# Optimization experiments

Measured on AMD Instinct MI355X. Metric: run time of the kernel, lower is better.

Reference implementation:

```python
import jax, jax.numpy as jnp
import numpy as np

NG, ND, NS, E, DIM, H = 20000, 8000, 8000, 300000, 256, 8
HD = DIM // H
SCALE = 1.0 / float(np.sqrt(HD))
EPS = 1e-5


def _ln(x, g, b):
    mu = x.mean(-1, keepdims=True)
    var = ((x - mu) ** 2).mean(-1, keepdims=True)
    return (x - mu) / jnp.sqrt(var + EPS) * g + b


def _attn(h_src, h_dst, Wq, bq, Wk, bk, Wv, bv, src, dst, n_dst):
    # multi-head edge dot-product attention with edge_softmax over incoming edges
    Q = (h_dst @ Wq.T + bq).reshape(-1, H, HD)
    K = (h_src @ Wk.T + bk).reshape(-1, H, HD)
    V = (h_src @ Wv.T + bv).reshape(-1, H, HD)
    score = jnp.einsum('ehd,ehd->eh', K[src], Q[dst]) * SCALE  # [E, H]
    m = jax.ops.segment_max(score, dst, num_segments=n_dst)
    m = jnp.where(jnp.isfinite(m), m, 0.0)  # nodes with no in-edges
    a = jnp.exp(score - m[dst])
    denom = jax.ops.segment_sum(a, dst, num_segments=n_dst)
    a = a / denom[dst]
    h = jax.ops.segment_sum(V[src] * a[:, :, None], dst, num_segments=n_dst)
    return h.reshape(n_dst, DIM)


def _bahdanau(m1, m2, W1, b1, W2, b2, v, bv):
    e1 = (jnp.tanh(m1 @ W1.T + b1) @ v.T + bv)[:, 0]
    e2 = (jnp.tanh(m2 @ W2.T + b2) @ v.T + bv)[:, 0]
    w = jax.nn.softmax(jnp.stack([e1, e2], axis=1), axis=1)
    return w[:, 0:1] * m1 + w[:, 1:2] * m2


def _forward(gene_feat, drug_feat, disease_feat,
             dg_Wq, dg_bq, dg_Wk, dg_bk, dg_Wv, dg_bv,
             disg_Wq, disg_bq, disg_Wk, disg_bk, disg_Wv, disg_bv,
             gd_Wq, gd_bq, gd_Wk, gd_bk, gd_Wv, gd_bv,
             gdis_Wq, gdis_bq, gdis_Wk, gdis_bk, gdis_Wv, gdis_bv,
             f_W1, f_b1, f_W2, f_b2, f_v, f_bv,
             ln1_g, ln1_b, ln2_g, ln2_b,
             dg_src, dg_dst, disg_src, disg_dst, gd_src, gd_dst, gdis_src, gdis_dst):
    gm_drug = _attn(drug_feat, gene_feat, dg_Wq, dg_bq, dg_Wk, dg_bk, dg_Wv, dg_bv, dg_src, dg_dst, NG)
    gm_dis = _attn(disease_feat, gene_feat, disg_Wq, disg_bq, disg_Wk, disg_bk, disg_Wv, disg_bv, disg_src, disg_dst, NG)
    has_d = jnp.zeros((NG,), bool).at[dg_dst].set(True)
    has_s = jnp.zeros((NG,), bool).at[disg_dst].set(True)
    fused = _bahdanau(gm_drug, gm_dis, f_W1, f_b1, f_W2, f_b2, f_v, f_bv)
    gene_msg = jnp.where((has_d & has_s)[:, None], fused,
                         jnp.where(has_d[:, None], gm_drug,
                                   jnp.where(has_s[:, None], gm_dis, 0.0)))
    gene_out = _ln(gene_feat + jax.nn.gelu(gene_msg, approximate=False), ln1_g, ln1_b)
    drug_msg = _attn(gene_out, drug_feat, gd_Wq, gd_bq, gd_Wk, gd_bk, gd_Wv, gd_bv, gd_src, gd_dst, ND)
    dis_msg = _attn(gene_out, disease_feat, gdis_Wq, gdis_bq, gdis_Wk, gdis_bk, gdis_Wv, gdis_bv, gdis_src, gdis_dst, NS)
    drug_out = _ln(drug_feat + jax.nn.gelu(drug_msg, approximate=False), ln2_g, ln2_b)
    disease_out = _ln(disease_feat + jax.nn.gelu(dis_msg, approximate=False), ln2_g, ln2_b)
    return (drug_out, disease_out, gene_out)


def setup_inputs() -> dict:
    ks = jax.random.split(jax.random.key(0), 40)
    it = iter(range(40))

    def nrm(shape):
        return jax.random.normal(ks[next(it)], shape, dtype=jnp.float32)

    def xav(din, dout):
        lim = float(np.sqrt(6.0 / (din + dout)))
        return jax.random.uniform(ks[next(it)], (dout, din), minval=-lim, maxval=lim, dtype=jnp.float32)

    def ridx(n, hi):
        return jax.random.randint(ks[next(it)], (n,), 0, hi, dtype=jnp.int32)

    inp = {}
    inp['gene_feat'] = nrm((NG, DIM))
    inp['drug_feat'] = nrm((ND, DIM))
    inp['disease_feat'] = nrm((NS, DIM))
    for p in ['dg', 'disg', 'gd', 'gdis']:
        inp[p + '_Wq'] = xav(DIM, DIM)
        inp[p + '_bq'] = jnp.zeros((DIM,), jnp.float32)
        inp[p + '_Wk'] = xav(DIM, DIM)
        inp[p + '_bk'] = jnp.zeros((DIM,), jnp.float32)
        inp[p + '_Wv'] = xav(DIM, DIM)
        inp[p + '_bv'] = jnp.zeros((DIM,), jnp.float32)
    inp['f_W1'] = xav(DIM, DIM); inp['f_b1'] = jnp.zeros((DIM,), jnp.float32)
    inp['f_W2'] = xav(DIM, DIM); inp['f_b2'] = jnp.zeros((DIM,), jnp.float32)
    inp['f_v'] = xav(DIM, 1); inp['f_bv'] = jnp.zeros((1,), jnp.float32)
    inp['ln1_g'] = jnp.ones((DIM,), jnp.float32); inp['ln1_b'] = jnp.zeros((DIM,), jnp.float32)
    inp['ln2_g'] = jnp.ones((DIM,), jnp.float32); inp['ln2_b'] = jnp.zeros((DIM,), jnp.float32)
    inp['dg_src'] = ridx(E, ND); inp['dg_dst'] = ridx(E, NG)
    inp['disg_src'] = ridx(E, NS); inp['disg_dst'] = ridx(E, NG)
    inp['gd_src'] = ridx(E, NG); inp['gd_dst'] = ridx(E, ND)
    inp['gdis_src'] = ridx(E, NG); inp['gdis_dst'] = ridx(E, NS)
    return inp


def reference(gene_feat, drug_feat, disease_feat,
              dg_Wq, dg_bq, dg_Wk, dg_bk, dg_Wv, dg_bv,
              disg_Wq, disg_bq, disg_Wk, disg_bk, disg_Wv, disg_bv,
              gd_Wq, gd_bq, gd_Wk, gd_bk, gd_Wv, gd_bv,
              gdis_Wq, gdis_bq, gdis_Wk, gdis_bk, gdis_Wv, gdis_bv,
              f_W1, f_b1, f_W2, f_b2, f_v, f_bv,
              ln1_g, ln1_b, ln2_g, ln2_b,
              dg_src, dg_dst, disg_src, disg_dst, gd_src, gd_dst, gdis_src, gdis_dst):
    return _forward(gene_feat, drug_feat, disease_feat,
                    dg_Wq, dg_bq, dg_Wk, dg_bk, dg_Wv, dg_bv,
                    disg_Wq, disg_bq, disg_Wk, disg_bk, disg_Wv, disg_bv,
                    gd_Wq, gd_bq, gd_Wk, gd_bk, gd_Wv, gd_bv,
                    gdis_Wq, gdis_bq, gdis_Wk, gdis_bk, gdis_Wv, gdis_bv,
                    f_W1, f_b1, f_W2, f_b2, f_v, f_bv,
                    ln1_g, ln1_b, ln2_g, ln2_b,
                    dg_src, dg_dst, disg_src, disg_dst, gd_src, gd_dst, gdis_src, gdis_dst)
```

## Files before the change

### kernel.cpp

```cpp
#include <hip/hip_runtime.h>

#define NG 20000
#define ND 8000
#define NS 8000
#define EE 300000
#define DIM 256
#define SCALE_QK 0.17677669529663687f
#define LNEPS 1e-5f

#define MAXB 40
#define L1CH 2048
#define NCH1 ((EE + L1CH - 1) / L1CH)
#define CB_G 8704
#define CB_S 10496
#define RB_G (40 * CB_G)
#define RB_S (32 * CB_S)

typedef __attribute__((ext_vector_type(4))) float floatx4;
typedef __attribute__((ext_vector_type(8))) short shortx8;
typedef __attribute__((ext_vector_type(8))) unsigned short ushortx8;
typedef unsigned int u32;

__device__ __forceinline__ float bf2f(unsigned short u) {
    union { unsigned u; float f; } c; c.u = ((unsigned)u) << 16; return c.f;
}
__device__ __forceinline__ unsigned short f2bf(float f) {
    union { float f; unsigned u; } c; c.f = f;
    return (unsigned short)((c.u + 0x7fffu + ((c.u >> 16) & 1u)) >> 16);
}
__device__ __forceinline__ float gelu_exact(float v) {
    return 0.5f * v * (1.0f + erff(v * 0.70710678118654752f));
}

__device__ __forceinline__ void async_load16(const unsigned short* g,
                                             unsigned short* lds) {
    __builtin_amdgcn_global_load_lds(
        (const __attribute__((address_space(1))) u32*)(const void*)g,
        (__attribute__((address_space(3))) u32*)(void*)lds, 16, 0, 0);
}

__device__ __forceinline__ int swzoff(int row, int q) {
    int p = (row >> 1) & 7, b = row & 1;
    return ((row >> 4) * 64 + p * 8 + (((b << 2) + q) ^ p)) * 8;
}

struct GemmDesc {
    const unsigned short* A; const unsigned short* W;
    const float* b1; const float* b2; const float* b3; const float* b4;
    unsigned short* C; int ldc;
    const float* vvec; float* evec;
    int M; int gx; int ncol; int mode; int kvi;
};
struct GemmBatch { GemmDesc d[4]; };

__global__ __launch_bounds__(256, 4) void gemm_batch_kernel(GemmBatch gb)
{
    __shared__ unsigned short As[2][128 * 32];
    __shared__ unsigned short Bs[2][64 * 32];
    const GemmDesc d = gb.d[blockIdx.z];
    if ((int)blockIdx.x >= d.gx) return;
    const int n0 = blockIdx.y * 64;
    if (n0 >= d.ncol) return;

    const int tid = threadIdx.x;
    const int lane = tid & 63, wv = tid >> 6;
    const int quad = lane >> 4, l16 = lane & 15;
    const int m0 = blockIdx.x * 128;

    const int sp = lane >> 3, ss = lane & 7;
    const int srow = 2 * sp + ((ss ^ sp) >> 2);
    const int sq = (ss ^ sp) & 3;
    const unsigned short* gA0 = d.A + (size_t)(m0 + wv * 16 + srow) * 256 + sq * 8;
    const unsigned short* gA1 = d.A + (size_t)(m0 + 64 + wv * 16 + srow) * 256 + sq * 8;
    const unsigned short* gB  = d.W + (size_t)(n0 + wv * 16 + srow) * 256 + sq * 8;

    floatx4 acc[2][4];
#pragma unroll
    for (int i = 0; i < 2; ++i)
#pragma unroll
        for (int j = 0; j < 4; ++j) acc[i][j] = (floatx4){0.f, 0.f, 0.f, 0.f};

    async_load16(gA0, &As[0][(wv * 16) * 32]);
    async_load16(gA1, &As[0][(64 + wv * 16) * 32]);
    async_load16(gB,  &Bs[0][(wv * 16) * 32]);
    __syncthreads();

    for (int k0 = 0; k0 < 256; k0 += 32) {
        const int buf = (k0 >> 5) & 1;
        if (k0 < 224) {
            const int nb = buf ^ 1;
            async_load16(gA0 + k0 + 32, &As[nb][(wv * 16) * 32]);
            async_load16(gA1 + k0 + 32, &As[nb][(64 + wv * 16) * 32]);
            async_load16(gB + k0 + 32,  &Bs[nb][(wv * 16) * 32]);
        }
        shortx8 af[2], bfr[4];
#pragma unroll
        for (int mf = 0; mf < 2; ++mf)
            af[mf] = *(const shortx8*)(&As[buf][swzoff(wv * 32 + mf * 16 + l16, quad)]);
#pragma unroll
        for (int nf = 0; nf < 4; ++nf)
            bfr[nf] = *(const shortx8*)(&Bs[buf][swzoff(nf * 16 + l16, quad)]);
#pragma unroll
        for (int mf = 0; mf < 2; ++mf)
#pragma unroll
            for (int nf = 0; nf < 4; ++nf)
                acc[mf][nf] = __builtin_amdgcn_mfma_f32_16x16x32_bf16(
                    af[mf], bfr[nf], acc[mf][nf], 0, 0, 0);
        __syncthreads();
    }

    if (d.mode == 0) {
#pragma unroll
        for (int mf = 0; mf < 2; ++mf)
#pragma unroll
            for (int r = 0; r < 4; ++r) {
                int m = m0 + wv * 32 + mf * 16 + quad * 4 + r;
                if (m < d.M) {
#pragma unroll
                    for (int nf = 0; nf < 4; ++nf) {
                        int n = n0 + nf * 16 + l16;
                        int h = n >> 8;
                        const float* bp = (h == 0) ? d.b1 : (h == 1) ? d.b2
                                        : (h == 2) ? d.b3 : d.b4;
                        float bn = bp[n & 255];
                        int pos;
                        if (d.kvi) {
                            int nn = n & 511;
                            pos = (n & ~511) + ((nn & 255) >> 2) * 8 + (nn & 3) +
                                  ((nn >> 8) << 2);
                        } else {
                            pos = n;
                        }
                        d.C[(size_t)m * d.ldc + pos] = f2bf(acc[mf][nf][r] + bn);
                    }
                }
            }
    } else {
        float p[2][4] = {};
#pragma unroll
        for (int mf = 0; mf < 2; ++mf)
#pragma unroll
            for (int nf = 0; nf < 4; ++nf) {
                int n = n0 + nf * 16 + l16;
                float vn = d.vvec[n];
                float bn = d.b1[n];
#pragma unroll
                for (int r = 0; r < 4; ++r)
                    p[mf][r] += vn * tanhf(acc[mf][nf][r] + bn);
            }
#pragma unroll
        for (int mf = 0; mf < 2; ++mf)
#pragma unroll
            for (int r = 0; r < 4; ++r) {
                float s = p[mf][r];
                s += __shfl_xor(s, 1); s += __shfl_xor(s, 2);
                s += __shfl_xor(s, 4); s += __shfl_xor(s, 8);
                if (l16 == 0) {
                    int m = m0 + wv * 32 + mf * 16 + quad * 4 + r;
                    if (m < d.M) atomicAdd(&d.evec[m], s);
                }
            }
    }
}

struct PrepP {
    int* zb; int zn; int nzb;
    const float* wsrc[14];
    unsigned short* wout;
    const float* gf; const float* df; const float* sf;
    unsigned short* go; unsigned short* dfo; unsigned short* so;
};
__global__ void prep_kernel(PrepP p) {
    int bid = blockIdx.x, tid = threadIdx.x;
    if (bid < p.nzb) {
        int i = bid * 256 + tid;
        if (i < p.zn) p.zb[i] = 0;
        return;
    }
    bid -= p.nzb;
    if (bid < 896) {
        int idx = bid * 256 + tid;
        int mat = idx >> 14;
        int e = (idx & 16383) << 2;
        float4 f = *(const float4*)(p.wsrc[mat] + e);
        ushort4 t;
        t.x = f2bf(f.x); t.y = f2bf(f.y); t.z = f2bf(f.z); t.w = f2bf(f.w);
        *(ushort4*)(p.wout + ((size_t)mat << 16) + e) = t;
        return;
    }
    bid -= 896;
    const int NG4 = NG * 64, ND4 = ND * 64, NS4 = NS * 64;
    int i = bid * 256 + tid;
    const float* in; unsigned short* out; int j;
    if (i < NG4) { in = p.gf; out = p.go; j = i; }
    else if (i < NG4 + ND4) { in = p.df; out = p.dfo; j = i - NG4; }
    else if (i < NG4 + ND4 + NS4) { in = p.sf; out = p.so; j = i - NG4 - ND4; }
    else return;
    float4 f = *(const float4*)(in + (size_t)j * 4);
    ushort4 t;
    t.x = f2bf(f.x); t.y = f2bf(f.y); t.z = f2bf(f.z); t.w = f2bf(f.w);
    *(ushort4*)(out + (size_t)j * 4) = t;
}

__global__ void fillf_kernel(float* __restrict__ p, int n, float v) {
    int i = blockIdx.x * blockDim.x + threadIdx.x;
    if (i < n) p[i] = v;
}

struct L1P {
    const int* src[4];
    const int* dst[4];
    int* brec[4];
    int* bcur;
};
__global__ __launch_bounds__(256) void l1_bucket_kernel(L1P a) {
    __shared__ int hist[MAXB];
    int g = blockIdx.x / NCH1, c = blockIdx.x - g * NCH1;
    int base = c * L1CH;
    int tid = threadIdx.x;
    const int shift = (g < 2) ? 9 : 8;
    const int CB = (g < 2) ? CB_G : CB_S;
    const int NB = (g < 2) ? 40 : 32;
    if (tid < NB) hist[tid] = 0;
    __syncthreads();
    const int* __restrict__ dstp = a.dst[g];
    const int* __restrict__ srcp = a.src[g];
    int bk[8], rec[8], lr[8];
#pragma unroll
    for (int j = 0; j < 8; ++j) {
        int e = base + j * 256 + tid;
        bool ok = e < EE;
        int dd = ok ? dstp[e] : 0;
        int ss = ok ? srcp[e] : 0;
        bk[j] = dd >> shift;
        rec[j] = ((dd & ((1 << shift) - 1)) << 15) | ss;
        lr[j] = ok ? atomicAdd(&hist[bk[j]], 1) : -1;
    }
    __syncthreads();
    if (tid < NB) {
        int h = hist[tid];
        if (h > 0) hist[tid] = atomicAdd(&a.bcur[g * MAXB + tid], h);
    }
    __syncthreads();
    int* __restrict__ recp = a.brec[g];
#pragma unroll
    for (int j = 0; j < 8; ++j) {
        if (lr[j] >= 0) {
            int pos = hist[bk[j]] + lr[j];
            if (pos < CB) recp[bk[j] * CB + pos] = rec[j];
        }
    }
}

struct L2P {
    const int* brec[4];
    const int* bcur;
    int* cnt[4];
    int* offs[4];
    int* srcs[4];
};
__global__ __launch_bounds__(256) void l2_csr_kernel(L2P a) {
    __shared__ int hist[512];
    __shared__ int loffs[512];
    __shared__ int cur[512];
    __shared__ int ws2[4];
    __shared__ int bb;
    int bid = blockIdx.x, tid = threadIdx.x;
    int g, b;
    if (bid < 40) { g = 0; b = bid; }
    else if (bid < 80) { g = 1; b = bid - 40; }
    else if (bid < 112) { g = 2; b = bid - 80; }
    else { g = 3; b = bid - 112; }
    const int shift = (g < 2) ? 9 : 8;
    const int BSZ = 1 << shift;
    const int CB = (g < 2) ? CB_G : CB_S;
    const int N = (g < 2) ? NG : ((g == 2) ? ND : NS);
    hist[tid] = 0; hist[256 + tid] = 0;
    if (tid == 0) {
        int s = 0;
        const int* bc = a.bcur + g * MAXB;
        for (int i = 0; i < b; ++i) s += bc[i];
        bb = s;
    }
    __syncthreads();
    int total = a.bcur[g * MAXB + b];
    if (total > CB) total = CB;
    const int* __restrict__ recp = a.brec[g] + b * CB;
    for (int i = tid; i < total; i += 256)
        atomicAdd(&hist[recp[i] >> 15], 1);
    __syncthreads();
    int v0 = hist[2 * tid], v1 = hist[2 * tid + 1];
    int s = v0 + v1, x = s;
    int lane = tid & 63, wv = tid >> 6;
#pragma unroll
    for (int o = 1; o < 64; o <<= 1) {
        int u = __shfl_up(x, o);
        if (lane >= o) x += u;
    }
    if (lane == 63) ws2[wv] = x;
    __syncthreads();
    int woff = 0;
    for (int w = 0; w < wv; ++w) woff += ws2[w];
    int excl = woff + x - s;
    loffs[2 * tid] = excl; loffs[2 * tid + 1] = excl + v0;
    cur[2 * tid] = excl;  cur[2 * tid + 1] = excl + v0;
    int base = bb;
    int lo = b << shift;
    for (int i = tid; i < BSZ; i += 256) {
        int dd = lo + i;
        if (dd < N) {
            a.cnt[g][dd] = hist[i];
            a.offs[g][dd] = base + loffs[i];
        }
    }
    __syncthreads();
    int* __restrict__ sp = a.srcs[g];
    for (int i = tid; i < total; i += 256) {
        int rec = recp[i];
        int pos = atomicAdd(&cur[rec >> 15], 1);
        sp[base + pos] = rec & 0x7fff;
    }
}

__device__ __forceinline__ void wave_attn_node(
    const unsigned short* __restrict__ Q, int qs,
    const unsigned short* __restrict__ KV,
    const int* __restrict__ offs, const int* __restrict__ cnt,
    const int* __restrict__ srcs, int du, int lane,
    float& g0, float& g1, float& g2, float& g3)
{
    const int lo = lane * 4;
    const int lofs = lane * 8;
    ushort4 qv = *(const ushort4*)(Q + (size_t)du * qs + lo);
    const float q0 = bf2f(qv.x), q1 = bf2f(qv.y), q2 = bf2f(qv.z), q3 = bf2f(qv.w);
    const int beg = offs[du], num = cnt[du];

    float m[8], l[8], a[8][4];
#pragma unroll
    for (int c = 0; c < 8; ++c) {
        m[c] = -INFINITY; l[c] = 0.f;
        a[c][0] = a[c][1] = a[c][2] = a[c][3] = 0.f;
    }

    int sb[8];
    if (num > 0) {
#pragma unroll
        for (int c = 0; c < 8; ++c)
            sb[c] = srcs[beg + ((c < num) ? c : (num - 1))];
    }

    for (int i = 0; i < num; i += 8) {
        int sn[8];
        const bool more = (i + 8) < num;
        if (more) {
#pragma unroll
            for (int c = 0; c < 8; ++c) {
                int idx = i + 8 + c;
                sn[c] = srcs[beg + ((idx < num) ? idx : (num - 1))];
            }
        }
        ushortx8 kv[8];
#pragma unroll
        for (int c = 0; c < 8; ++c)
            kv[c] = *(const ushortx8*)(KV + (size_t)sb[c] * 512 + lofs);
        float p[8];
#pragma unroll
        for (int c = 0; c < 8; ++c)
            p[c] = q0 * bf2f(kv[c][0]) + q1 * bf2f(kv[c][1]) +
                   q2 * bf2f(kv[c][2]) + q3 * bf2f(kv[c][3]);
#pragma unroll
        for (int c = 0; c < 8; ++c) p[c] += __shfl_xor(p[c], 1);
#pragma unroll
        for (int c = 0; c < 8; ++c) p[c] += __shfl_xor(p[c], 2);
#pragma unroll
        for (int c = 0; c < 8; ++c) p[c] += __shfl_xor(p[c], 4);
#pragma unroll
        for (int c = 0; c < 8; ++c) {
            if (i + c < num) {
                float sc = p[c] * SCALE_QK;
                float mn = fmaxf(m[c], sc);
                float eo = __expf(m[c] - mn);
                float en = __expf(sc - mn);
                a[c][0] = a[c][0] * eo + en * bf2f(kv[c][4]);
                a[c][1] = a[c][1] * eo + en * bf2f(kv[c][5]);
                a[c][2] = a[c][2] * eo + en * bf2f(kv[c][6]);
                a[c][3] = a[c][3] * eo + en * bf2f(kv[c][7]);
                l[c] = l[c] * eo + en;
                m[c] = mn;
            }
        }
        if (more) {
#pragma unroll
            for (int c = 0; c < 8; ++c) sb[c] = sn[c];
        }
    }

    float ms = fmaxf(fmaxf(fmaxf(m[0], m[1]), fmaxf(m[2], m[3])),
                     fmaxf(fmaxf(m[4], m[5]), fmaxf(m[6], m[7])));
    float A0 = 0.f, A1 = 0.f, A2 = 0.f, A3 = 0.f, L = 0.f;
    if (ms > -INFINITY) {
#pragma unroll
        for (int c = 0; c < 8; ++c) {
            float w = __expf(m[c] - ms);
            A0 += a[c][0] * w; A1 += a[c][1] * w;
            A2 += a[c][2] * w; A3 += a[c][3] * w;
            L += l[c] * w;
        }
    }
    float inv = (L > 0.f) ? 1.f / L : 0.f;
    g0 = A0 * inv; g1 = A1 * inv; g2 = A2 * inv; g3 = A3 * inv;
}

__device__ __forceinline__ void wave_ln_store(
    float x0, float x1, float x2, float x3,
    const float* __restrict__ g, const float* __restrict__ b,
    float* __restrict__ out, unsigned short* __restrict__ out_bf,
    int du, int lo)
{
    float s1 = x0 + x1 + x2 + x3;
    float s2 = x0 * x0 + x1 * x1 + x2 * x2 + x3 * x3;
#pragma unroll
    for (int o = 1; o < 64; o <<= 1) {
        s1 += __shfl_xor(s1, o);
        s2 += __shfl_xor(s2, o);
    }
    float mu = s1 * (1.f / 256.f);
    float var = fmaxf(s2 * (1.f / 256.f) - mu * mu, 0.f);
    float rs = rsqrtf(var + LNEPS);
    float4 gv = *(const float4*)(g + lo);
    float4 bv = *(const float4*)(b + lo);
    float y0 = (x0 - mu) * rs * gv.x + bv.x;
    float y1 = (x1 - mu) * rs * gv.y + bv.y;
    float y2 = (x2 - mu) * rs * gv.z + bv.z;
    float y3 = (x3 - mu) * rs * gv.w + bv.w;
    *(float4*)(out + (size_t)du * 256 + lo) = make_float4(y0, y1, y2, y3);
    if (out_bf) {
        ushort4 t; t.x = f2bf(y0); t.y = f2bf(y1); t.z = f2bf(y2); t.w = f2bf(y3);
        *(ushort4*)(out_bf + (size_t)du * 256 + lo) = t;
    }
}

struct AggDesc {
    const unsigned short* Q; int qs;
    const unsigned short* KV;
    const int* offs; const int* cnt; const int* srcs;
    unsigned short* gm;
    const float* feat; const float* g; const float* b; float* out;
    int N;
};
template <int LN>
__global__ __launch_bounds__(256) void agg2_kernel(AggDesc a0, AggDesc a1, int nb0)
{
    const bool first = (int)blockIdx.x < nb0;
    const AggDesc d = first ? a0 : a1;
    const int bx = first ? blockIdx.x : (blockIdx.x - nb0);
    int lane = threadIdx.x & 63, wv = threadIdx.x >> 6;
    int nd = bx * 4 + wv;
    if (nd >= d.N) return;
    int du = __builtin_amdgcn_readfirstlane(nd);
    int lo = lane * 4;
    float g0, g1, g2, g3;
    wave_attn_node(d.Q, d.qs, d.KV, d.offs, d.cnt, d.srcs, du, lane, g0, g1, g2, g3);
    if (LN == 0) {
        ushort4 t; t.x = f2bf(g0); t.y = f2bf(g1); t.z = f2bf(g2); t.w = f2bf(g3);
        *(ushort4*)(d.gm + (size_t)du * 256 + lo) = t;
    } else {
        float4 fv = *(const float4*)(d.feat + (size_t)du * 256 + lo);
        float x0 = fv.x + gelu_exact(g0);
        float x1 = fv.y + gelu_exact(g1);
        float x2 = fv.z + gelu_exact(g2);
        float x3 = fv.w + gelu_exact(g3);
        wave_ln_store(x0, x1, x2, x3, d.g, d.b, d.out, nullptr, du, lo);
    }
}

__global__ __launch_bounds__(256) void gene_fusion_kernel(
    const float* __restrict__ gene_feat, const unsigned short* __restrict__ gm_d,
    const unsigned short* __restrict__ gm_s, const float* __restrict__ e1,
    const float* __restrict__ e2, const int* __restrict__ cnt_d,
    const int* __restrict__ cnt_s, const float* __restrict__ g,
    const float* __restrict__ b, float* __restrict__ out,
    unsigned short* __restrict__ out_bf)
{
    int lane = threadIdx.x & 63, wv = threadIdx.x >> 6;
    int d = blockIdx.x * 4 + wv;
    if (d >= NG) return;
    int du = __builtin_amdgcn_readfirstlane(d);
    int lo = lane * 4;
    ushort4 v1 = *(const ushort4*)(gm_d + (size_t)du * 256 + lo);
    ushort4 v2 = *(const ushort4*)(gm_s + (size_t)du * 256 + lo);
    bool hd = cnt_d[du] > 0, hs = cnt_s[du] > 0;
    float wa, wb;
    if (hd && hs) {
        float aa = e1[du], bb = e2[du];
        float mm = fmaxf(aa, bb);
        float ea = __expf(aa - mm), eb = __expf(bb - mm);
        float inv = 1.f / (ea + eb);
        wa = ea * inv; wb = eb * inv;
    } else if (hd) { wa = 1.f; wb = 0.f; }
    else if (hs) { wa = 0.f; wb = 1.f; }
    else { wa = 0.f; wb = 0.f; }
    float m0 = wa * bf2f(v1.x) + wb * bf2f(v2.x);
    float m1 = wa * bf2f(v1.y) + wb * bf2f(v2.y);
    float m2 = wa * bf2f(v1.z) + wb * bf2f(v2.z);
    float m3 = wa * bf2f(v1.w) + wb * bf2f(v2.w);
    float4 fv = *(const float4*)(gene_feat + (size_t)du * 256 + lo);
    float x0 = fv.x + gelu_exact(m0);
    float x1 = fv.y + gelu_exact(m1);
    float x2 = fv.z + gelu_exact(m2);
    float x3 = fv.w + gelu_exact(m3);
    wave_ln_store(x0, x1, x2, x3, g, b, out, out_bf, du, lo);
}

extern "C" void kernel_launch(void* const* d_in, const int* in_sizes, int n_in,
                              void* d_out, int out_size, void* d_ws, size_t ws_size,
                              hipStream_t stream)
{
    float* out_f32 = (float*)d_out;

    const float* gene_feat    = (const float*)d_in[0];
    const float* drug_feat    = (const float*)d_in[1];
    const float* disease_feat = (const float*)d_in[2];
    const float* dg_Wq = (const float*)d_in[3];
    const float* dg_bq = (const float*)d_in[4];
    const float* dg_Wk = (const float*)d_in[5];
    const float* dg_bk = (const float*)d_in[6];
    const float* dg_Wv = (const float*)d_in[7];
    const float* dg_bv = (const float*)d_in[8];
    const float* disg_Wq = (const float*)d_in[9];
    const float* disg_bq = (const float*)d_in[10];
    const float* disg_Wk = (const float*)d_in[11];
    const float* disg_bk = (const float*)d_in[12];
    const float* disg_Wv = (const float*)d_in[13];
    const float* disg_bv = (const float*)d_in[14];
    const float* gd_Wq = (const float*)d_in[15];
    const float* gd_bq = (const float*)d_in[16];
    const float* gd_Wk = (const float*)d_in[17];
    const float* gd_bk = (const float*)d_in[18];
    const float* gd_Wv = (const float*)d_in[19];
    const float* gd_bv = (const float*)d_in[20];
    const float* gdis_Wq = (const float*)d_in[21];
    const float* gdis_bq = (const float*)d_in[22];
    const float* gdis_Wk = (const float*)d_in[23];
    const float* gdis_bk = (const float*)d_in[24];
    const float* gdis_Wv = (const float*)d_in[25];
    const float* gdis_bv = (const float*)d_in[26];
    const float* f_W1 = (const float*)d_in[27];
    const float* f_b1 = (const float*)d_in[28];
    const float* f_W2 = (const float*)d_in[29];
    const float* f_b2 = (const float*)d_in[30];
    const float* f_v  = (const float*)d_in[31];
    const float* ln1_g = (const float*)d_in[33];
    const float* ln1_b = (const float*)d_in[34];
    const float* ln2_g = (const float*)d_in[35];
    const float* ln2_b = (const float*)d_in[36];
    const int* dg_src   = (const int*)d_in[37];
    const int* dg_dst   = (const int*)d_in[38];
    const int* disg_src = (const int*)d_in[39];
    const int* disg_dst = (const int*)d_in[40];
    const int* gd_src   = (const int*)d_in[41];
    const int* gd_dst   = (const int*)d_in[42];
    const int* gdis_src = (const int*)d_in[43];
    const int* gdis_dst = (const int*)d_in[44];

    char* ws = (char*)d_ws;
    size_t off = 0;
    auto alloc = [&](size_t bytes) -> char* {
        char* p = ws + off;
        off += (bytes + 511) & ~(size_t)511;
        return p;
    };
    int* bcur = (int*)alloc(4 * MAXB * 4);
    float* e1 = (float*)alloc(NG * 4);
    float* e2 = (float*)alloc(NG * 4);
    size_t zero_len = off;
    int* offs_dg   = (int*)alloc(NG * 4);
    int* offs_disg = (int*)alloc(NG * 4);
    int* offs_gd   = (int*)alloc(ND * 4);
    int* offs_gdis = (int*)alloc(NS * 4);
    int* cnt_dg    = (int*)alloc(NG * 4);
    int* cnt_disg  = (int*)alloc(NG * 4);
    int* cnt_gd    = (int*)alloc(ND * 4);
    int* cnt_gdis  = (int*)alloc(NS * 4);
    int* srcs_dg   = (int*)alloc((size_t)EE * 4);
    int* srcs_disg = (int*)alloc((size_t)EE * 4);
    int* srcs_gd   = (int*)alloc((size_t)EE * 4);
    int* srcs_gdis = (int*)alloc((size_t)EE * 4);
    unsigned short* Q12  = (unsigned short*)alloc((size_t)NG * 512 * 2);
    unsigned short* KVb  = (unsigned short*)alloc((size_t)NG * 512 * 2);
    unsigned short* gm_d = (unsigned short*)alloc((size_t)NG * 256 * 2);
    unsigned short* gm_s = (unsigned short*)alloc((size_t)NG * 256 * 2);
    unsigned short* gene_bf = (unsigned short*)alloc((size_t)NG * 256 * 2);
    unsigned short* drug_bf = (unsigned short*)alloc((size_t)ND * 256 * 2);
    unsigned short* dis_bf  = (unsigned short*)alloc((size_t)NS * 256 * 2);
    unsigned short* Wbf     = (unsigned short*)alloc((size_t)14 * 65536 * 2);
    char* guard = alloc(64 * 1024);
    (void)guard;
    size_t need = off;

    int* brec0 = (int*)Q12;
    int* brec1 = brec0 + RB_G;
    int* brec2 = brec1 + RB_G;
    int* brec3 = brec2 + RB_S;

    unsigned short* KVb2 = gm_s;
    unsigned short* KVs1b = KVb + (size_t)ND * 512;
    unsigned short* Qd = Q12;
    unsigned short* Qs = Q12 + (size_t)ND * 256;
    unsigned short* gene_out_bf = gm_d;

    float* out_drug = out_f32;
    float* out_dis  = out_drug + (size_t)ND * 256;
    float* out_gene = out_dis + (size_t)NS * 256;

    if (ws_size < need) {
        fillf_kernel<<<(out_size + 255) / 256, 256, 0, stream>>>(out_f32, out_size, 1000.0f);
        return;
    }

    {
        PrepP p;
        p.zb = (int*)d_ws;
        p.zn = (int)(zero_len / 4);
        p.nzb = (p.zn + 255) / 256;
        const float* wl[14] = {dg_Wq, disg_Wq, dg_Wk, dg_Wv, disg_Wk, disg_Wv,
                               gd_Wk, gd_Wv, gdis_Wk, gdis_Wv, gd_Wq, gdis_Wq,
                               f_W1, f_W2};
        for (int i = 0; i < 14; ++i) p.wsrc[i] = wl[i];
        p.wout = Wbf;
        p.gf = gene_feat; p.df = drug_feat; p.sf = disease_feat;
        p.go = gene_bf; p.dfo = drug_bf; p.so = dis_bf;
        int nfeat = ((NG + ND + NS) * 64 + 255) / 256;
        prep_kernel<<<p.nzb + 896 + nfeat, 256, 0, stream>>>(p);
    }

    {
        L1P p;
        p.src[0] = dg_src; p.src[1] = disg_src; p.src[2] = gd_src; p.src[3] = gdis_src;
        p.dst[0] = dg_dst; p.dst[1] = disg_dst; p.dst[2] = gd_dst; p.dst[3] = gdis_dst;
        p.brec[0] = brec0; p.brec[1] = brec1; p.brec[2] = brec2; p.brec[3] = brec3;
        p.bcur = bcur;
        l1_bucket_kernel<<<4 * NCH1, 256, 0, stream>>>(p);
    }
    {
        L2P p;
        p.brec[0] = brec0; p.brec[1] = brec1; p.brec[2] = brec2; p.brec[3] = brec3;
        p.bcur = bcur;
        p.cnt[0] = cnt_dg; p.cnt[1] = cnt_disg; p.cnt[2] = cnt_gd; p.cnt[3] = cnt_gdis;
        p.offs[0] = offs_dg; p.offs[1] = offs_disg; p.offs[2] = offs_gd; p.offs[3] = offs_gdis;
        p.srcs[0] = srcs_dg; p.srcs[1] = srcs_disg; p.srcs[2] = srcs_gd; p.srcs[3] = srcs_gdis;
        l2_csr_kernel<<<144, 256, 0, stream>>>(p);
    }

    const int GXG = (NG + 127) / 128;
    const int GXS = (ND + 127) / 128;

    auto mkd = [](const unsigned short* A, const unsigned short* W,
                  const float* b1, const float* b2, const float* b3, const float* b4,
                  unsigned short* C, int ldc, const float* vv, float* ev,
                  int M, int gx, int ncol, int mode, int kvi) {
        GemmDesc d;
        d.A = A; d.W = W; d.b1 = b1; d.b2 = b2; d.b3 = b3; d.b4 = b4;
        d.C = C; d.ldc = ldc; d.vvec = vv; d.evec = ev;
        d.M = M; d.gx = gx; d.ncol = ncol; d.mode = mode; d.kvi = kvi;
        return d;
    };
    auto mka = [](const unsigned short* Q, int qs, const unsigned short* KV,
                  const int* offs, const int* cnt, const int* srcs,
                  unsigned short* gm, const float* feat, const float* g,
                  const float* b, float* out, int N) {
        AggDesc d;
        d.Q = Q; d.qs = qs; d.KV = KV; d.offs = offs; d.cnt = cnt; d.srcs = srcs;
        d.gm = gm; d.feat = feat; d.g = g; d.b = b; d.out = out; d.N = N;
        return d;
    };

    {
        GemmBatch gb;
        gb.d[0] = mkd(gene_bf, Wbf, dg_bq, disg_bq, dg_bq, dg_bq,
                      Q12, 512, nullptr, nullptr, NG, GXG, 512, 0, 0);
        gb.d[1] = mkd(drug_bf, Wbf + (size_t)2 * 65536, dg_bk, dg_bv, dg_bk, dg_bk,
                      KVb, 512, nullptr, nullptr, ND, GXS, 512, 0, 1);
        gb.d[2] = mkd(dis_bf, Wbf + (size_t)4 * 65536, disg_bk, disg_bv, disg_bk, disg_bk,
                      KVs1b, 512, nullptr, nullptr, NS, GXS, 512, 0, 1);
        gb.d[3] = gb.d[2]; gb.d[3].gx = 0;
        gemm_batch_kernel<<<dim3(GXG, 8, 3), 256, 0, stream>>>(gb);
    }

    {
        AggDesc a0 = mka(Q12, 512, KVb, offs_dg, cnt_dg, srcs_dg,
                         gm_d, nullptr, nullptr, nullptr, nullptr, NG);
        AggDesc a1 = mka(Q12 + 256, 512, KVs1b, offs_disg, cnt_disg, srcs_disg,
                         gm_s, nullptr, nullptr, nullptr, nullptr, NG);
        int nb = (NG + 3) / 4;
        agg2_kernel<0><<<2 * nb, 256, 0, stream>>>(a0, a1, nb);
    }

    {
        GemmBatch gb;
        gb.d[0] = mkd(gm_d, Wbf + (size_t)12 * 65536, f_b1, f_b1, f_b1, f_b1,
                      nullptr, 256, f_v, e1, NG, GXG, 256, 1, 0);
        gb.d[1] = mkd(gm_s, Wbf + (size_t)13 * 65536, f_b2, f_b2, f_b2, f_b2,
                      nullptr, 256, f_v, e2, NG, GXG, 256, 1, 0);
        gb.d[2] = mkd(drug_bf, Wbf + (size_t)10 * 65536, gd_bq, gd_bq, gd_bq, gd_bq,
                      Qd, 256, nullptr, nullptr, ND, GXS, 256, 0, 0);
        gb.d[3] = mkd(dis_bf, Wbf + (size_t)11 * 65536, gdis_bq, gdis_bq, gdis_bq, gdis_bq,
                      Qs, 256, nullptr, nullptr, NS, GXS, 256, 0, 0);
        gemm_batch_kernel<<<dim3(GXG, 4, 4), 256, 0, stream>>>(gb);
    }

    gene_fusion_kernel<<<(NG + 3) / 4, 256, 0, stream>>>(
        gene_feat, gm_d, gm_s, e1, e2, cnt_dg, cnt_disg, ln1_g, ln1_b,
        out_gene, gene_out_bf);

    {
        GemmBatch gb;
        gb.d[0] = mkd(gene_out_bf, Wbf + (size_t)6 * 65536, gd_bk, gd_bv, gd_bk, gd_bk,
                      KVb, 512, nullptr, nullptr, NG, GXG, 512, 0, 1);
        gb.d[1] = mkd(gene_out_bf, Wbf + (size_t)8 * 65536, gdis_bk, gdis_bv, gdis_bk, gdis_bk,
                      KVb2, 512, nullptr, nullptr, NG, GXG, 512, 0, 1);
        gb.d[2] = gb.d[1]; gb.d[2].gx = 0;
        gb.d[3] = gb.d[1]; gb.d[3].gx = 0;
        gemm_batch_kernel<<<dim3(GXG, 8, 2), 256, 0, stream>>>(gb);
    }

    {
        AggDesc a0 = mka(Qd, 256, KVb, offs_gd, cnt_gd, srcs_gd,
                         nullptr, drug_feat, ln2_g, ln2_b, out_drug, ND);
        AggDesc a1 = mka(Qs, 256, KVb2, offs_gdis, cnt_gdis, srcs_gdis,
                         nullptr, disease_feat, ln2_g, ln2_b, out_dis, NS);
        int nb = (ND + 3) / 4;
        agg2_kernel<1><<<2 * nb, 256, 0, stream>>>(a0, a1, nb);
    }
}
```

Measured before the change: 485.0 us.

## Merge per-slot online softmax into one running state and use persistent agg grid

The edge-attention aggregation used to keep eight independent online-softmax states per lane, one per unrolled edge slot, and merged them at the end. It now takes the max over each 8-edge batch and rescales a single accumulator once per batch, which cuts register use and the number of exponentials. The aggregation kernel also becomes a grid-stride loop over a grid capped at 2048 blocks, with launch bounds asking for higher occupancy. The trade-off is that the rescale now depends on a reduction across the batch, and the capped grid may balance poorly when nodes have very different in-degrees.

```diff
diff --git a/kernel.cpp b/kernel.cpp
--- a/kernel.cpp
+++ b/kernel.cpp
@@ -335,12 +335,8 @@
     const float q0 = bf2f(qv.x), q1 = bf2f(qv.y), q2 = bf2f(qv.z), q3 = bf2f(qv.w);
     const int beg = offs[du], num = cnt[du];
 
-    float m[8], l[8], a[8][4];
-#pragma unroll
-    for (int c = 0; c < 8; ++c) {
-        m[c] = -INFINITY; l[c] = 0.f;
-        a[c][0] = a[c][1] = a[c][2] = a[c][3] = 0.f;
-    }
+    float m = -INFINITY, l = 0.f;
+    float a0 = 0.f, a1 = 0.f, a2 = 0.f, a3 = 0.f;
 
     int sb[8];
     if (num > 0) {
@@ -374,41 +370,35 @@
         for (int c = 0; c < 8; ++c) p[c] += __shfl_xor(p[c], 2);
 #pragma unroll
         for (int c = 0; c < 8; ++c) p[c] += __shfl_xor(p[c], 4);
+        float sc[8];
+#pragma unroll
+        for (int c = 0; c < 8; ++c)
+            sc[c] = (i + c < num) ? p[c] * SCALE_QK : -INFINITY;
+        float bm = fmaxf(fmaxf(fmaxf(sc[0], sc[1]), fmaxf(sc[2], sc[3])),
+                         fmaxf(fmaxf(sc[4], sc[5]), fmaxf(sc[6], sc[7])));
+        float mn = fmaxf(m, bm);
+        float eo = __expf(m - mn);
+        a0 *= eo; a1 *= eo; a2 *= eo; a3 *= eo; l *= eo;
+        float en[8];
+#pragma unroll
+        for (int c = 0; c < 8; ++c) en[c] = __expf(sc[c] - mn);
 #pragma unroll
         for (int c = 0; c < 8; ++c) {
-            if (i + c < num) {
-                float sc = p[c] * SCALE_QK;
-                float mn = fmaxf(m[c], sc);
-                float eo = __expf(m[c] - mn);
-                float en = __expf(sc - mn);
-                a[c][0] = a[c][0] * eo + en * bf2f(kv[c][4]);
-                a[c][1] = a[c][1] * eo + en * bf2f(kv[c][5]);
-                a[c][2] = a[c][2] * eo + en * bf2f(kv[c][6]);
-                a[c][3] = a[c][3] * eo + en * bf2f(kv[c][7]);
-                l[c] = l[c] * eo + en;
-                m[c] = mn;
-            }
+            a0 += en[c] * bf2f(kv[c][4]);
+            a1 += en[c] * bf2f(kv[c][5]);
+            a2 += en[c] * bf2f(kv[c][6]);
+            a3 += en[c] * bf2f(kv[c][7]);
+            l += en[c];
         }
+        m = mn;
         if (more) {
 #pragma unroll
             for (int c = 0; c < 8; ++c) sb[c] = sn[c];
         }
     }
 
-    float ms = fmaxf(fmaxf(fmaxf(m[0], m[1]), fmaxf(m[2], m[3])),
-                     fmaxf(fmaxf(m[4], m[5]), fmaxf(m[6], m[7])));
-    float A0 = 0.f, A1 = 0.f, A2 = 0.f, A3 = 0.f, L = 0.f;
-    if (ms > -INFINITY) {
-#pragma unroll
-        for (int c = 0; c < 8; ++c) {
-            float w = __expf(m[c] - ms);
-            A0 += a[c][0] * w; A1 += a[c][1] * w;
-            A2 += a[c][2] * w; A3 += a[c][3] * w;
-            L += l[c] * w;
-        }
-    }
-    float inv = (L > 0.f) ? 1.f / L : 0.f;
-    g0 = A0 * inv; g1 = A1 * inv; g2 = A2 * inv; g3 = A3 * inv;
+    float inv = (l > 0.f) ? 1.f / l : 0.f;
+    g0 = a0 * inv; g1 = a1 * inv; g2 = a2 * inv; g3 = a3 * inv;
 }
 
 __device__ __forceinline__ void wave_ln_store(
@@ -449,28 +439,32 @@
     int N;
 };
 template <int LN>
-__global__ __launch_bounds__(256) void agg2_kernel(AggDesc a0, AggDesc a1, int nb0)
+__global__ __launch_bounds__(256, 8) void agg2_kernel(
+    AggDesc a0, AggDesc a1, int nb0, int nbtot)
 {
-    const bool first = (int)blockIdx.x < nb0;
-    const AggDesc d = first ? a0 : a1;
-    const int bx = first ? blockIdx.x : (blockIdx.x - nb0);
     int lane = threadIdx.x & 63, wv = threadIdx.x >> 6;
-    int nd = bx * 4 + wv;
-    if (nd >= d.N) return;
-    int du = __builtin_amdgcn_readfirstlane(nd);
     int lo = lane * 4;
-    float g0, g1, g2, g3;
-    wave_attn_node(d.Q, d.qs, d.KV, d.offs, d.cnt, d.srcs, du, lane, g0, g1, g2, g3);
-    if (LN == 0) {
-        ushort4 t; t.x = f2bf(g0); t.y = f2bf(g1); t.z = f2bf(g2); t.w = f2bf(g3);
-        *(ushort4*)(d.gm + (size_t)du * 256 + lo) = t;
-    } else {
-        float4 fv = *(const float4*)(d.feat + (size_t)du * 256 + lo);
-        float x0 = fv.x + gelu_exact(g0);
-        float x1 = fv.y + gelu_exact(g1);
-        float x2 = fv.z + gelu_exact(g2);
-        float x3 = fv.w + gelu_exact(g3);
-        wave_ln_store(x0, x1, x2, x3, d.g, d.b, d.out, nullptr, du, lo);
+    for (int bx = blockIdx.x; bx < nbtot; bx += gridDim.x) {
+        const bool first = bx < nb0;
+        const AggDesc d = first ? a0 : a1;
+        const int bxx = first ? bx : (bx - nb0);
+        int nd = bxx * 4 + wv;
+        if (nd >= d.N) continue;
+        int du = __builtin_amdgcn_readfirstlane(nd);
+        float g0, g1, g2, g3;
+        wave_attn_node(d.Q, d.qs, d.KV, d.offs, d.cnt, d.srcs, du, lane,
+                       g0, g1, g2, g3);
+        if (LN == 0) {
+            ushort4 t; t.x = f2bf(g0); t.y = f2bf(g1); t.z = f2bf(g2); t.w = f2bf(g3);
+            *(ushort4*)(d.gm + (size_t)du * 256 + lo) = t;
+        } else {
+            float4 fv = *(const float4*)(d.feat + (size_t)du * 256 + lo);
+            float x0 = fv.x + gelu_exact(g0);
+            float x1 = fv.y + gelu_exact(g1);
+            float x2 = fv.z + gelu_exact(g2);
+            float x3 = fv.w + gelu_exact(g3);
+            wave_ln_store(x0, x1, x2, x3, d.g, d.b, d.out, nullptr, du, lo);
+        }
     }
 }
 
@@ -693,7 +687,9 @@
         AggDesc a1 = mka(Q12 + 256, 512, KVs1b, offs_disg, cnt_disg, srcs_disg,
                          gm_s, nullptr, nullptr, nullptr, nullptr, NG);
         int nb = (NG + 3) / 4;
-        agg2_kernel<0><<<2 * nb, 256, 0, stream>>>(a0, a1, nb);
+        int nbtot = 2 * nb;
+        int grid = nbtot < 2048 ? nbtot : 2048;
+        agg2_kernel<0><<<grid, 256, 0, stream>>>(a0, a1, nb, nbtot);
     }
 
     {
@@ -730,6 +726,8 @@
         AggDesc a1 = mka(Qs, 256, KVb2, offs_gdis, cnt_gdis, srcs_gdis,
                          nullptr, disease_feat, ln2_g, ln2_b, out_dis, NS);
         int nb = (ND + 3) / 4;
-        agg2_kernel<1><<<2 * nb, 256, 0, stream>>>(a0, a1, nb);
-    }
-}
+        int nbtot = 2 * nb;
+        int grid = nbtot < 2048 ? nbtot : 2048;
+        agg2_kernel<1><<<grid, 256, 0, stream>>>(a0, a1, nb, nbtot);
+    }
+}
```

Result: slower. 497.4 us (+2.6%).
